# Performance work log

Measured on AMD Instinct MI355X. Metric: run time of the kernel, lower is better.

## Reference

```python
import jax, jax.numpy as jnp
import numpy as np

NUM_HEADS = 16

def setup_inputs() -> dict:
    key = jax.random.key(0)
    ks = jax.random.split(key, 6)
    B, S, D = 2, 2048, 1024
    x = jax.random.normal(ks[0], (B, S, D), dtype=jnp.float32)
    s = 1.0 / np.sqrt(D)
    Wq = jax.random.normal(ks[1], (D, D), dtype=jnp.float32) * s
    Wk = jax.random.normal(ks[2], (D, D), dtype=jnp.float32) * s
    Wv = jax.random.normal(ks[3], (D, D), dtype=jnp.float32) * s
    Wff = jax.random.normal(ks[4], (D, D), dtype=jnp.float32) * s
    bff = jax.random.normal(ks[5], (D,), dtype=jnp.float32) * 0.01
    return {"x": x, "Wq": Wq, "Wk": Wk, "Wv": Wv, "Wff": Wff, "bff": bff}

def reference(x, Wq, Wk, Wv, Wff, bff):
    B, S, D = x.shape
    H = NUM_HEADS
    Dh = D // H
    # Q/K/V projections (bias-free Linears). Original scales Q by 1/sqrt(hidden_size).
    q = (x @ Wq.T) * (1.0 / jnp.sqrt(jnp.asarray(D, x.dtype)))
    k = x @ Wk.T
    v = x @ Wv.T
    q = q.reshape(B, S, H, Dh)
    k = k.reshape(B, S, H, Dh)
    v = v.reshape(B, S, H, Dh)
    # Blockwise online-softmax attention is mathematically identical to
    # full softmax attention over all keys (no causal mask in source).
    scores = jnp.einsum('bqhd,bkhd->bhqk', q, k)
    attn = jax.nn.softmax(scores, axis=-1)
    out = jnp.einsum('bhqk,bkhd->bqhd', attn, v).reshape(B, S, D)
    # Final feedforward Linear(hidden, hidden) with bias.
    return out @ Wff.T + bff
```

## Files before the change

### kernel.cpp

```cpp
#include <hip/hip_runtime.h>
#include <stdint.h>

typedef __attribute__((ext_vector_type(8))) short bf16x8;
typedef __attribute__((ext_vector_type(4))) float f32x4;

__device__ __forceinline__ uint16_t f2bf(float f) {
  union { float f; uint32_t u; } a; a.f = f;
  uint32_t u = a.u;
  u += 0x7FFFu + ((u >> 16) & 1u);
  return (uint16_t)(u >> 16);
}

__device__ __forceinline__ uint32_t pk_bf16(float a, float b) {
#if __has_builtin(__builtin_amdgcn_cvt_pk_bf16_f32)
  auto r = __builtin_amdgcn_cvt_pk_bf16_f32(a, b);
  uint32_t u; __builtin_memcpy(&u, &r, sizeof(u));
  return u;
#else
  return (uint32_t)f2bf(a) | ((uint32_t)f2bf(b) << 16);
#endif
}

__device__ __forceinline__ uint32_t pk_bf16_fast(float a, float b) {
#if __has_builtin(__builtin_amdgcn_cvt_pk_bf16_f32)
  auto r = __builtin_amdgcn_cvt_pk_bf16_f32(a, b);
  uint32_t u; __builtin_memcpy(&u, &r, sizeof(u));
  return u;
#else
  uint32_t ua, ub;
  __builtin_memcpy(&ua, &a, 4); __builtin_memcpy(&ub, &b, 4);
  return __builtin_amdgcn_perm(ub, ua, 0x07060302u);
#endif
}

__device__ __forceinline__ float fast_exp2(float x) {
#if __has_builtin(__builtin_amdgcn_exp2f)
  return __builtin_amdgcn_exp2f(x);
#else
  return exp2f(x);
#endif
}

__device__ __forceinline__ void gld_lds16(const uint16_t* g, uint16_t* l) {
  __builtin_amdgcn_global_load_lds(
      (const __attribute__((address_space(1))) void*)g,
      (__attribute__((address_space(3))) void*)l, 16, 0, 0);
}

__global__ void cast_all(const float* __restrict__ x, const float* __restrict__ wq,
                         const float* __restrict__ wk, const float* __restrict__ wv,
                         const float* __restrict__ wff,
                         uint16_t* __restrict__ xb, uint16_t* __restrict__ wqb,
                         uint16_t* __restrict__ wkb, uint16_t* __restrict__ wvb,
                         uint16_t* __restrict__ wffb) {
  int i = blockIdx.x * blockDim.x + threadIdx.x;
  const float* src; uint16_t* dst; int off;
  if (i < 1048576)      { src = x;   dst = xb;   off = i; }
  else if (i < 1310720) { src = wq;  dst = wqb;  off = i - 1048576; }
  else if (i < 1572864) { src = wk;  dst = wkb;  off = i - 1310720; }
  else if (i < 1835008) { src = wv;  dst = wvb;  off = i - 1572864; }
  else                  { src = wff; dst = wffb; off = i - 1835008; }
  float4 v = ((const float4*)src)[off];
  uint2 o; o.x = pk_bf16(v.x, v.y); o.y = pk_bf16(v.z, v.w);
  ((uint2*)dst)[off] = o;
}

__device__ __forceinline__ void gemm_tile(const uint16_t* __restrict__ Abase,
                                          const uint16_t* __restrict__ Bbase,
                                          uint16_t* lds, f32x4 acc[4][4]) {
  const int tid  = threadIdx.x;
  const int w    = tid >> 6;
  const int lane = tid & 63;
  const int wm   = w >> 1, wn = w & 1;
  const int lrow = lane & 15;
  const int quad = lane >> 4;
  const int srow = lane >> 3;
  const int lc   = (lane & 7) ^ srow;
  const int sx   = lrow & 7;
  uint16_t* a_lds = lds;
  uint16_t* b_lds = lds + 8192;

#pragma unroll
  for (int mt = 0; mt < 4; ++mt)
#pragma unroll
    for (int nt = 0; nt < 4; ++nt)
      acc[mt][nt] = (f32x4){0.f, 0.f, 0.f, 0.f};

  const uint16_t* ag = Abase + (size_t)(w * 32 + srow) * 1024 + lc * 8;
  const uint16_t* bg = Bbase + (size_t)(w * 32 + srow) * 1024 + lc * 8;

  for (int k0 = 0; k0 < 1024; k0 += 64) {
#pragma unroll
    for (int i8 = 0; i8 < 4; ++i8) {
      gld_lds16(ag + (size_t)i8 * 8 * 1024 + k0, a_lds + (w * 4 + i8) * 512);
      gld_lds16(bg + (size_t)i8 * 8 * 1024 + k0, b_lds + (w * 4 + i8) * 512);
    }
    __syncthreads();
#pragma unroll
    for (int ks = 0; ks < 2; ++ks) {
      bf16x8 af[4], bfr[4];
      const int c = ((ks * 4 + quad) ^ sx) << 3;
#pragma unroll
      for (int mt = 0; mt < 4; ++mt)
        af[mt] = *(const bf16x8*)(a_lds + (wm * 64 + mt * 16 + lrow) * 64 + c);
#pragma unroll
      for (int nt = 0; nt < 4; ++nt)
        bfr[nt] = *(const bf16x8*)(b_lds + (wn * 64 + nt * 16 + lrow) * 64 + c);
#pragma unroll
      for (int mt = 0; mt < 4; ++mt)
#pragma unroll
        for (int nt = 0; nt < 4; ++nt)
          acc[mt][nt] = __builtin_amdgcn_mfma_f32_16x16x32_bf16(af[mt], bfr[nt], acc[mt][nt], 0, 0, 0);
    }
    __syncthreads();
  }
}

__global__ __launch_bounds__(256) void gemm_qkv(
    const uint16_t* __restrict__ x,
    const uint16_t* __restrict__ wq, const uint16_t* __restrict__ wk, const uint16_t* __restrict__ wv,
    uint16_t* __restrict__ qo, uint16_t* __restrict__ ko, uint16_t* __restrict__ vto) {
  __shared__ __align__(16) uint16_t lds[17408];
  const int bx = blockIdx.x;
  const int mi = ((bx & 7) << 2) + (bx >> 3);
  const int m0 = mi * 128, n0 = blockIdx.y * 128, z = blockIdx.z;
  f32x4 acc[4][4];
  if (z < 2) {
    const uint16_t* W = (z == 0) ? wq : wk;
    gemm_tile(W + (size_t)n0 * 1024, x + (size_t)m0 * 1024, lds, acc);
  } else {
    gemm_tile(x + (size_t)m0 * 1024, wv + (size_t)n0 * 1024, lds, acc);
  }

  const int tid = threadIdx.x;
  const int lane = tid & 63, w = tid >> 6;
  const int wm = w >> 1, wn = w & 1, lrow = lane & 15, quad = lane >> 4;
  const float scale = (z == 0) ? 0.045084222f : 1.0f;

#pragma unroll
  for (int mt = 0; mt < 4; ++mt)
#pragma unroll
    for (int nt = 0; nt < 4; ++nt) {
      int i0 = wm * 64 + mt * 16 + quad * 4;
      int j  = wn * 64 + nt * 16 + lrow;
      uint2 dd;
      dd.x = pk_bf16(acc[mt][nt][0] * scale, acc[mt][nt][1] * scale);
      dd.y = pk_bf16(acc[mt][nt][2] * scale, acc[mt][nt][3] * scale);
      *(uint2*)(&lds[j * 136 + i0]) = dd;
    }
  __syncthreads();

  uint16_t* outp = (z == 0) ? qo : (z == 1) ? ko : vto;
  if (z < 2) {
#pragma unroll
    for (int it = 0; it < 8; ++it) {
      int idx = it * 256 + tid;
      int jj = idx >> 4, cc = idx & 15;
      uint4 v = *(const uint4*)(&lds[jj * 136 + cc * 8]);
      int m = m0 + jj, n = n0 + cc * 8;
      int b = m >> 11, s = m & 2047, h = n >> 6, dh = n & 63;
      *(uint4*)(outp + ((size_t)((b * 16 + h) * 2048 + s)) * 64 + dh) = v;
    }
  } else {
    int b = m0 >> 11, sbase = m0 & 2047;
#pragma unroll
    for (int it = 0; it < 8; ++it) {
      int idx = it * 256 + tid;
      int ff = idx >> 4, cc = idx & 15;
      uint4 v = *(const uint4*)(&lds[ff * 136 + cc * 8]);
      int n = n0 + ff, h = n >> 6, dh = n & 63;
      *(uint4*)(outp + ((size_t)((b * 16 + h) * 64 + dh)) * 2048 + sbase + cc * 8) = v;
    }
  }
}

__global__ __launch_bounds__(256) void gemm_ff(
    const uint16_t* __restrict__ ao, const uint16_t* __restrict__ wff,
    const float* __restrict__ bff, float* __restrict__ out) {
  __shared__ __align__(16) uint16_t lds[12288];
  const int bx = blockIdx.x;
  const int mi = ((bx & 7) << 2) + (bx >> 3);
  const int m0 = mi * 128, n0 = blockIdx.y * 64;
  const int tid  = threadIdx.x;
  const int w    = tid >> 6;
  const int lane = tid & 63;
  const int wm   = w >> 1, wn = w & 1;
  const int lrow = lane & 15;
  const int quad = lane >> 4;
  const int srow = lane >> 3;
  const int lc   = (lane & 7) ^ srow;
  const int sx   = lrow & 7;
  uint16_t* a_lds = lds;
  uint16_t* b_lds = lds + 4096;

  f32x4 acc[4][2];
#pragma unroll
  for (int mt = 0; mt < 4; ++mt)
#pragma unroll
    for (int nt = 0; nt < 2; ++nt)
      acc[mt][nt] = (f32x4){0.f, 0.f, 0.f, 0.f};

  const uint16_t* ag = wff + (size_t)(n0 + w * 16 + srow) * 1024 + lc * 8;
  const uint16_t* bg = ao  + (size_t)(m0 + w * 32 + srow) * 1024 + lc * 8;

  for (int k0 = 0; k0 < 1024; k0 += 64) {
#pragma unroll
    for (int i2 = 0; i2 < 2; ++i2)
      gld_lds16(ag + (size_t)i2 * 8 * 1024 + k0, a_lds + (w * 2 + i2) * 512);
#pragma unroll
    for (int i8 = 0; i8 < 4; ++i8)
      gld_lds16(bg + (size_t)i8 * 8 * 1024 + k0, b_lds + (w * 4 + i8) * 512);
    __syncthreads();
#pragma unroll
    for (int ks = 0; ks < 2; ++ks) {
      bf16x8 af[2], bfr[4];
      const int c = ((ks * 4 + quad) ^ sx) << 3;
#pragma unroll
      for (int nt = 0; nt < 2; ++nt)
        af[nt] = *(const bf16x8*)(a_lds + (wn * 32 + nt * 16 + lrow) * 64 + c);
#pragma unroll
      for (int mt = 0; mt < 4; ++mt)
        bfr[mt] = *(const bf16x8*)(b_lds + (wm * 64 + mt * 16 + lrow) * 64 + c);
#pragma unroll
      for (int mt = 0; mt < 4; ++mt)
#pragma unroll
        for (int nt = 0; nt < 2; ++nt)
          acc[mt][nt] = __builtin_amdgcn_mfma_f32_16x16x32_bf16(af[nt], bfr[mt], acc[mt][nt], 0, 0, 0);
    }
    __syncthreads();
  }

  float* fl = (float*)lds;
#pragma unroll
  for (int p = 0; p < 2; ++p) {
    if (wm == p) {
#pragma unroll
      for (int mt = 0; mt < 4; ++mt)
#pragma unroll
        for (int nt = 0; nt < 2; ++nt)
          *(f32x4*)(&fl[(mt * 16 + lrow) * 68 + wn * 32 + nt * 16 + quad * 4]) = acc[mt][nt];
    }
    __syncthreads();
#pragma unroll
    for (int it = 0; it < 4; ++it) {
      int idx = it * 256 + tid;
      int jj = idx >> 4, cc = idx & 15;
      f32x4 v = *(const f32x4*)(&fl[jj * 68 + cc * 4]);
      int n = n0 + cc * 4;
      f32x4 bias = *(const f32x4*)(bff + n);
      f32x4 vv = v + bias;
      *(f32x4*)(out + (size_t)(m0 + p * 64 + jj) * 1024 + n) = vv;
    }
    __syncthreads();
  }
}

__global__ __launch_bounds__(512, 4) void attn(
    const uint16_t* __restrict__ q, const uint16_t* __restrict__ k,
    const uint16_t* __restrict__ vt, uint16_t* __restrict__ ao) {
  __shared__ __align__(16) uint16_t lds_all[32768];
  uint16_t* const k_lds = lds_all;
  uint16_t* const v_lds = lds_all + 8192;
  uint16_t* const p_lds = lds_all + 16384;
  const int tid = threadIdx.x, w = tid >> 6, lane = tid & 63;
  const int lrow = lane & 15, quad = lane >> 4;
  const int srow = lane >> 3, lc = (lane & 7) ^ srow, sx = lrow & 7;
  const int kw = w & 3, qw = w >> 2;
  const int pk = w & 1, pq = w >> 1;
  const int pswz = (lrow & 7) << 1;

  const int lin = blockIdx.x + (blockIdx.y << 4);
  const int wl  = ((lin & 7) << 6) + (lin >> 3);
  const int qb  = wl & 15, bh = wl >> 4;

  const uint16_t* Q = q  + (size_t)bh * (2048 * 64);
  const uint16_t* K = k  + (size_t)bh * (2048 * 64);
  const uint16_t* V = vt + (size_t)bh * (64 * 2048);

  const int qr0 = qb * 128;
  bf16x8 qf[4][2];
#pragma unroll
  for (int qh = 0; qh < 4; ++qh)
#pragma unroll
    for (int ks = 0; ks < 2; ++ks)
      qf[qh][ks] = *(const bf16x8*)(Q + (size_t)(qr0 + qw * 64 + qh * 16 + lrow) * 64 + ks * 32 + quad * 8);

  f32x4 o[2][4];
#pragma unroll
  for (int qh2 = 0; qh2 < 2; ++qh2)
#pragma unroll
    for (int dt = 0; dt < 4; ++dt) o[qh2][dt] = (f32x4){0.f, 0.f, 0.f, 0.f};
  float ls[4] = {0.f, 0.f, 0.f, 0.f};
  bf16x8 vfr[4];

  auto stage = [&](int kb, int bi) {
    gld_lds16(K + (size_t)(kb * 64 + w * 8 + srow) * 64 + lc * 8, k_lds + bi * 4096 + w * 512);
    gld_lds16(V + (size_t)(w * 8 + srow) * 2048 + kb * 64 + lc * 8, v_lds + bi * 4096 + w * 512);
  };
  stage(0, 0);

  for (int kb = 0; kb < 32; ++kb) {
    const int bi = kb & 1;
    __syncthreads();

    if (kb > 0) {
      const uint16_t* pbuf = p_lds + (bi ^ 1) * 8192;
      __builtin_amdgcn_s_setprio(1);
#pragma unroll
      for (int qh2 = 0; qh2 < 2; ++qh2) {
        int row = pq * 32 + qh2 * 16 + lrow;
        bf16x8 pa = *(const bf16x8*)(pbuf + row * 64 + (((pk * 8 + quad * 2) ^ pswz) << 2));
#pragma unroll
        for (int dt = 0; dt < 4; ++dt)
          o[qh2][dt] = __builtin_amdgcn_mfma_f32_16x16x32_bf16(vfr[dt], pa, o[qh2][dt], 0, 0, 0);
      }
      __builtin_amdgcn_s_setprio(0);
    }

#pragma unroll
    for (int dt = 0; dt < 4; ++dt)
      vfr[dt] = *(const bf16x8*)(v_lds + bi * 4096 + (dt * 16 + lrow) * 64 + (((pk * 4 + quad) ^ sx) << 3));

    if (kb + 1 < 32) stage(kb + 1, bi ^ 1);

    f32x4 s[4];
#pragma unroll
    for (int qh = 0; qh < 4; ++qh) s[qh] = (f32x4){0.f, 0.f, 0.f, 0.f};
    __builtin_amdgcn_s_setprio(1);
#pragma unroll
    for (int ks = 0; ks < 2; ++ks) {
      bf16x8 kf = *(const bf16x8*)(k_lds + bi * 4096 + (kw * 16 + lrow) * 64 + (((ks * 4 + quad) ^ sx) << 3));
#pragma unroll
      for (int qh = 0; qh < 4; ++qh)
        s[qh] = __builtin_amdgcn_mfma_f32_16x16x32_bf16(kf, qf[qh][ks], s[qh], 0, 0, 0);
    }
    __builtin_amdgcn_s_setprio(0);

    uint16_t* pbw = p_lds + bi * 8192;
#pragma unroll
    for (int qh = 0; qh < 4; ++qh) {
      float p0 = fast_exp2(s[qh][0]);
      float p1 = fast_exp2(s[qh][1]);
      float p2 = fast_exp2(s[qh][2]);
      float p3 = fast_exp2(s[qh][3]);
      ls[qh] += (p0 + p1) + (p2 + p3);
      uint2 dd; dd.x = pk_bf16_fast(p0, p1); dd.y = pk_bf16_fast(p2, p3);
      int row = qw * 64 + qh * 16 + lrow;
      *(uint2*)(pbw + row * 64 + (((kw * 4 + quad) ^ pswz) << 2)) = dd;
    }
  }

  __syncthreads();
  {
    const uint16_t* pbuf = p_lds + 8192;
    __builtin_amdgcn_s_setprio(1);
#pragma unroll
    for (int qh2 = 0; qh2 < 2; ++qh2) {
      int row = pq * 32 + qh2 * 16 + lrow;
      bf16x8 pa = *(const bf16x8*)(pbuf + row * 64 + (((pk * 8 + quad * 2) ^ pswz) << 2));
#pragma unroll
      for (int dt = 0; dt < 4; ++dt)
        o[qh2][dt] = __builtin_amdgcn_mfma_f32_16x16x32_bf16(vfr[dt], pa, o[qh2][dt], 0, 0, 0);
    }
    __builtin_amdgcn_s_setprio(0);
  }
  __syncthreads();

#pragma unroll
  for (int qh = 0; qh < 4; ++qh) {
    ls[qh] += __shfl_xor(ls[qh], 16);
    ls[qh] += __shfl_xor(ls[qh], 32);
  }
  float* arena = (float*)lds_all;
  float* lred  = (float*)(lds_all + 17408);
  if (quad == 0) {
#pragma unroll
    for (int qh = 0; qh < 4; ++qh) lred[kw * 128 + qw * 64 + qh * 16 + lrow] = ls[qh];
  }
  if (pk == 1) {
#pragma unroll
    for (int qh2 = 0; qh2 < 2; ++qh2)
#pragma unroll
      for (int dt = 0; dt < 4; ++dt)
        *(f32x4*)(&arena[(pq * 32 + qh2 * 16 + lrow) * 68 + dt * 16 + quad * 4]) = o[qh2][dt];
  }
  __syncthreads();

  if (pk == 0) {
    const int b = bh >> 4, h = bh & 15;
#pragma unroll
    for (int qh2 = 0; qh2 < 2; ++qh2) {
      int qrow = pq * 32 + qh2 * 16 + lrow;
      float l = lred[qrow] + lred[128 + qrow] + lred[256 + qrow] + lred[384 + qrow];
      float inv = 1.0f / l;
      int sg = qr0 + qrow;
#pragma unroll
      for (int dt = 0; dt < 4; ++dt) {
        f32x4 a = *(const f32x4*)(&arena[qrow * 68 + dt * 16 + quad * 4]);
        uint2 dd;
        dd.x = pk_bf16((o[qh2][dt][0] + a[0]) * inv, (o[qh2][dt][1] + a[1]) * inv);
        dd.y = pk_bf16((o[qh2][dt][2] + a[2]) * inv, (o[qh2][dt][3] + a[3]) * inv);
        *(uint2*)(ao + (size_t)(b * 2048 + sg) * 1024 + h * 64 + dt * 16 + quad * 4) = dd;
      }
    }
  }
}

extern "C" void kernel_launch(void* const* d_in, const int* in_sizes, int n_in,
                              void* d_out, int out_size, void* d_ws, size_t ws_size,
                              hipStream_t stream) {
  const float* x   = (const float*)d_in[0];
  const float* Wq  = (const float*)d_in[1];
  const float* Wk  = (const float*)d_in[2];
  const float* Wv  = (const float*)d_in[3];
  const float* Wff = (const float*)d_in[4];
  const float* bff = (const float*)d_in[5];
  float* out = (float*)d_out;

  uint16_t* ws = (uint16_t*)d_ws;
  uint16_t* x_bf   = ws;
  uint16_t* wq_bf  = ws + 4194304;
  uint16_t* wk_bf  = ws + 5242880;
  uint16_t* wv_bf  = ws + 6291456;
  uint16_t* wff_bf = ws + 7340032;
  uint16_t* q_bf   = ws + 8388608;
  uint16_t* k_bf   = ws + 12582912;
  uint16_t* vt_bf  = ws + 16777216;
  uint16_t* ao_bf  = ws + 20971520;

  cast_all<<<8192, 256, 0, stream>>>(x, Wq, Wk, Wv, Wff, x_bf, wq_bf, wk_bf, wv_bf, wff_bf);

  gemm_qkv<<<dim3(32, 8, 3), 256, 0, stream>>>(x_bf, wq_bf, wk_bf, wv_bf, q_bf, k_bf, vt_bf);
  attn<<<dim3(16, 32), 512, 0, stream>>>(q_bf, k_bf, vt_bf, ao_bf);
  gemm_ff<<<dim3(32, 16), 256, 0, stream>>>(ao_bf, wff_bf, bff, out);
}
```

Baseline: 173.7 us.

## Shrink attention key tile to 32 and split output dims across waves

The attention kernel moves from 64-key blocks to 32-key blocks, which cuts LDS use from 64KB to 40KB per block and raises the launch-bounds occupancy hint from 4 to 6. Waves are repartitioned so each one owns 32 query rows and half of the head dimension. This removes the cross-wave reduction of partial outputs through LDS and the matching arena writes and reads. The trade-off is twice as many loop iterations and barriers, plus a more complex staggered staging of K and V loads, in exchange for less LDS per block and higher occupancy.

```diff
diff --git a/kernel.cpp b/kernel.cpp
--- a/kernel.cpp
+++ b/kernel.cpp
@@ -255,19 +255,17 @@
   }
 }
 
-__global__ __launch_bounds__(512, 4) void attn(
+__global__ __launch_bounds__(512, 6) void attn(
     const uint16_t* __restrict__ q, const uint16_t* __restrict__ k,
     const uint16_t* __restrict__ vt, uint16_t* __restrict__ ao) {
-  __shared__ __align__(16) uint16_t lds_all[32768];
+  __shared__ __align__(16) uint16_t lds_all[20480];
   uint16_t* const k_lds = lds_all;
-  uint16_t* const v_lds = lds_all + 8192;
-  uint16_t* const p_lds = lds_all + 16384;
+  uint16_t* const v_lds = lds_all + 4096;
+  uint16_t* const p_lds = lds_all + 12288;
   const int tid = threadIdx.x, w = tid >> 6, lane = tid & 63;
   const int lrow = lane & 15, quad = lane >> 4;
   const int srow = lane >> 3, lc = (lane & 7) ^ srow, sx = lrow & 7;
-  const int kw = w & 3, qw = w >> 2;
-  const int pk = w & 1, pq = w >> 1;
-  const int pswz = (lrow & 7) << 1;
+  const int kt = w & 1, qg = w >> 1;
 
   const int lin = blockIdx.x + (blockIdx.y << 4);
   const int wl  = ((lin & 7) << 6) + (lin >> 3);
@@ -278,129 +276,131 @@
   const uint16_t* V = vt + (size_t)bh * (64 * 2048);
 
   const int qr0 = qb * 128;
-  bf16x8 qf[4][2];
-#pragma unroll
-  for (int qh = 0; qh < 4; ++qh)
+  bf16x8 qf[2][2];
+#pragma unroll
+  for (int qh = 0; qh < 2; ++qh)
 #pragma unroll
     for (int ks = 0; ks < 2; ++ks)
-      qf[qh][ks] = *(const bf16x8*)(Q + (size_t)(qr0 + qw * 64 + qh * 16 + lrow) * 64 + ks * 32 + quad * 8);
-
-  f32x4 o[2][4];
-#pragma unroll
-  for (int qh2 = 0; qh2 < 2; ++qh2)
-#pragma unroll
-    for (int dt = 0; dt < 4; ++dt) o[qh2][dt] = (f32x4){0.f, 0.f, 0.f, 0.f};
-  float ls[4] = {0.f, 0.f, 0.f, 0.f};
-  bf16x8 vfr[4];
-
-  auto stage = [&](int kb, int bi) {
-    gld_lds16(K + (size_t)(kb * 64 + w * 8 + srow) * 64 + lc * 8, k_lds + bi * 4096 + w * 512);
-    gld_lds16(V + (size_t)(w * 8 + srow) * 2048 + kb * 64 + lc * 8, v_lds + bi * 4096 + w * 512);
-  };
-  stage(0, 0);
-
-  for (int kb = 0; kb < 32; ++kb) {
-    const int bi = kb & 1;
-    __syncthreads();
+      qf[qh][ks] = *(const bf16x8*)(Q + (size_t)(qr0 + qg * 32 + qh * 16 + lrow) * 64 + ks * 32 + quad * 8);
+
+  f32x4 o[2][2];
+#pragma unroll
+  for (int qh = 0; qh < 2; ++qh)
+#pragma unroll
+    for (int dtl = 0; dtl < 2; ++dtl) o[qh][dtl] = (f32x4){0.f, 0.f, 0.f, 0.f};
+  float ls[2] = {0.f, 0.f};
+  bf16x8 vfr[2];
+
+  if (w < 4)
+    gld_lds16(K + (size_t)(0 * 32 + w * 8 + srow) * 64 + lc * 8, k_lds + 0 * 2048 + w * 512);
+  gld_lds16(V + (size_t)(w * 8 + srow) * 2048 + 0 * 64 + lc * 8, v_lds + 0 * 4096 + w * 512);
+
+  for (int kb = 0; kb < 64; ++kb) {
+    const int pb   = kb & 1;
+    const int vb   = (kb >> 1) & 1;
+    const int kbuf = kb & 1;
+    __syncthreads();
+
+    if (kb + 1 < 64 && w < 4)
+      gld_lds16(K + (size_t)((kb + 1) * 32 + w * 8 + srow) * 64 + lc * 8,
+                k_lds + ((kb + 1) & 1) * 2048 + w * 512);
+    {
+      const int vtile = (kb >> 1) + 1;
+      if (vtile < 32 && w >= 4) {
+        const int seg = (kb & 1) * 4 + (w - 4);
+        gld_lds16(V + (size_t)(seg * 8 + srow) * 2048 + vtile * 64 + lc * 8,
+                  v_lds + (vtile & 1) * 4096 + seg * 512);
+      }
+    }
 
     if (kb > 0) {
-      const uint16_t* pbuf = p_lds + (bi ^ 1) * 8192;
+      const uint16_t* pbuf = p_lds + (pb ^ 1) * 4096;
       __builtin_amdgcn_s_setprio(1);
 #pragma unroll
-      for (int qh2 = 0; qh2 < 2; ++qh2) {
-        int row = pq * 32 + qh2 * 16 + lrow;
-        bf16x8 pa = *(const bf16x8*)(pbuf + row * 64 + (((pk * 8 + quad * 2) ^ pswz) << 2));
-#pragma unroll
-        for (int dt = 0; dt < 4; ++dt)
-          o[qh2][dt] = __builtin_amdgcn_mfma_f32_16x16x32_bf16(vfr[dt], pa, o[qh2][dt], 0, 0, 0);
+      for (int qh = 0; qh < 2; ++qh) {
+        int row = qg * 32 + qh * 16 + lrow;
+        bf16x8 pa = *(const bf16x8*)(pbuf + row * 32 + ((quad ^ ((row >> 1) & 3)) << 3));
+#pragma unroll
+        for (int dtl = 0; dtl < 2; ++dtl)
+          o[qh][dtl] = __builtin_amdgcn_mfma_f32_16x16x32_bf16(vfr[dtl], pa, o[qh][dtl], 0, 0, 0);
       }
       __builtin_amdgcn_s_setprio(0);
     }
 
 #pragma unroll
-    for (int dt = 0; dt < 4; ++dt)
-      vfr[dt] = *(const bf16x8*)(v_lds + bi * 4096 + (dt * 16 + lrow) * 64 + (((pk * 4 + quad) ^ sx) << 3));
-
-    if (kb + 1 < 32) stage(kb + 1, bi ^ 1);
-
-    f32x4 s[4];
-#pragma unroll
-    for (int qh = 0; qh < 4; ++qh) s[qh] = (f32x4){0.f, 0.f, 0.f, 0.f};
+    for (int dtl = 0; dtl < 2; ++dtl)
+      vfr[dtl] = *(const bf16x8*)(v_lds + vb * 4096 + (kt * 32 + dtl * 16 + lrow) * 64
+                                  + ((((kb & 1) * 4 + quad) ^ sx) << 3));
+
+    f32x4 s[2];
+#pragma unroll
+    for (int qh = 0; qh < 2; ++qh) s[qh] = (f32x4){0.f, 0.f, 0.f, 0.f};
     __builtin_amdgcn_s_setprio(1);
 #pragma unroll
     for (int ks = 0; ks < 2; ++ks) {
-      bf16x8 kf = *(const bf16x8*)(k_lds + bi * 4096 + (kw * 16 + lrow) * 64 + (((ks * 4 + quad) ^ sx) << 3));
-#pragma unroll
-      for (int qh = 0; qh < 4; ++qh)
+      bf16x8 kf = *(const bf16x8*)(k_lds + kbuf * 2048 + (kt * 16 + lrow) * 64 + (((ks * 4 + quad) ^ sx) << 3));
+#pragma unroll
+      for (int qh = 0; qh < 2; ++qh)
         s[qh] = __builtin_amdgcn_mfma_f32_16x16x32_bf16(kf, qf[qh][ks], s[qh], 0, 0, 0);
     }
     __builtin_amdgcn_s_setprio(0);
 
-    uint16_t* pbw = p_lds + bi * 8192;
-#pragma unroll
-    for (int qh = 0; qh < 4; ++qh) {
+    uint16_t* pbw = p_lds + pb * 4096;
+#pragma unroll
+    for (int qh = 0; qh < 2; ++qh) {
       float p0 = fast_exp2(s[qh][0]);
       float p1 = fast_exp2(s[qh][1]);
       float p2 = fast_exp2(s[qh][2]);
       float p3 = fast_exp2(s[qh][3]);
       ls[qh] += (p0 + p1) + (p2 + p3);
       uint2 dd; dd.x = pk_bf16_fast(p0, p1); dd.y = pk_bf16_fast(p2, p3);
-      int row = qw * 64 + qh * 16 + lrow;
-      *(uint2*)(pbw + row * 64 + (((kw * 4 + quad) ^ pswz) << 2)) = dd;
+      int row = qg * 32 + qh * 16 + lrow;
+      *(uint2*)(pbw + row * 32 + (((kt * 4 + quad) ^ (lrow & 6)) << 2)) = dd;
     }
   }
 
   __syncthreads();
   {
-    const uint16_t* pbuf = p_lds + 8192;
+    const uint16_t* pbuf = p_lds + 4096;
     __builtin_amdgcn_s_setprio(1);
 #pragma unroll
-    for (int qh2 = 0; qh2 < 2; ++qh2) {
-      int row = pq * 32 + qh2 * 16 + lrow;
-      bf16x8 pa = *(const bf16x8*)(pbuf + row * 64 + (((pk * 8 + quad * 2) ^ pswz) << 2));
-#pragma unroll
-      for (int dt = 0; dt < 4; ++dt)
-        o[qh2][dt] = __builtin_amdgcn_mfma_f32_16x16x32_bf16(vfr[dt], pa, o[qh2][dt], 0, 0, 0);
+    for (int qh = 0; qh < 2; ++qh) {
+      int row = qg * 32 + qh * 16 + lrow;
+      bf16x8 pa = *(const bf16x8*)(pbuf + row * 32 + ((quad ^ ((row >> 1) & 3)) << 3));
+#pragma unroll
+      for (int dtl = 0; dtl < 2; ++dtl)
+        o[qh][dtl] = __builtin_amdgcn_mfma_f32_16x16x32_bf16(vfr[dtl], pa, o[qh][dtl], 0, 0, 0);
     }
     __builtin_amdgcn_s_setprio(0);
   }
   __syncthreads();
 
 #pragma unroll
-  for (int qh = 0; qh < 4; ++qh) {
+  for (int qh = 0; qh < 2; ++qh) {
     ls[qh] += __shfl_xor(ls[qh], 16);
     ls[qh] += __shfl_xor(ls[qh], 32);
   }
-  float* arena = (float*)lds_all;
-  float* lred  = (float*)(lds_all + 17408);
+  float* lred = (float*)lds_all;
   if (quad == 0) {
 #pragma unroll
-    for (int qh = 0; qh < 4; ++qh) lred[kw * 128 + qw * 64 + qh * 16 + lrow] = ls[qh];
-  }
-  if (pk == 1) {
-#pragma unroll
-    for (int qh2 = 0; qh2 < 2; ++qh2)
-#pragma unroll
-      for (int dt = 0; dt < 4; ++dt)
-        *(f32x4*)(&arena[(pq * 32 + qh2 * 16 + lrow) * 68 + dt * 16 + quad * 4]) = o[qh2][dt];
+    for (int qh = 0; qh < 2; ++qh) lred[kt * 128 + qg * 32 + qh * 16 + lrow] = ls[qh];
   }
   __syncthreads();
 
-  if (pk == 0) {
+  {
     const int b = bh >> 4, h = bh & 15;
 #pragma unroll
-    for (int qh2 = 0; qh2 < 2; ++qh2) {
-      int qrow = pq * 32 + qh2 * 16 + lrow;
-      float l = lred[qrow] + lred[128 + qrow] + lred[256 + qrow] + lred[384 + qrow];
+    for (int qh = 0; qh < 2; ++qh) {
+      int row = qg * 32 + qh * 16 + lrow;
+      float l = lred[row] + lred[128 + row];
       float inv = 1.0f / l;
-      int sg = qr0 + qrow;
-#pragma unroll
-      for (int dt = 0; dt < 4; ++dt) {
-        f32x4 a = *(const f32x4*)(&arena[qrow * 68 + dt * 16 + quad * 4]);
+      int sg = qr0 + row;
+#pragma unroll
+      for (int dtl = 0; dtl < 2; ++dtl) {
         uint2 dd;
-        dd.x = pk_bf16((o[qh2][dt][0] + a[0]) * inv, (o[qh2][dt][1] + a[1]) * inv);
-        dd.y = pk_bf16((o[qh2][dt][2] + a[2]) * inv, (o[qh2][dt][3] + a[3]) * inv);
-        *(uint2*)(ao + (size_t)(b * 2048 + sg) * 1024 + h * 64 + dt * 16 + quad * 4) = dd;
+        dd.x = pk_bf16(o[qh][dtl][0] * inv, o[qh][dtl][1] * inv);
+        dd.y = pk_bf16(o[qh][dtl][2] * inv, o[qh][dtl][3] * inv);
+        *(uint2*)(ao + (size_t)(b * 2048 + sg) * 1024 + h * 64 + kt * 32 + dtl * 16 + quad * 4) = dd;
       }
     }
   }
```

After: 175.9 us. No clear change (+1.3%).
